# Performance work log

Measured on AMD Instinct MI355X. Metric: run time of the kernel, lower is better.

## Reference

```python
import jax, jax.numpy as jnp
import numpy as np

N = 100000      # nodes
E = 6400000     # edges (avg degree 64)
S = 8           # FSM states
X = 2 ** S      # neighborhood 'characters' (256)
ITERS = 20      # NeuralFSM.iterations


def setup_inputs() -> dict:
    key = jax.random.key(0)
    k1, k2, k3 = jax.random.split(key, 3)
    # one-hot initial node states [N, S]
    state_idx = jax.random.randint(k1, (N,), 0, S)
    s0 = jax.nn.one_hot(state_idx, S, dtype=jnp.float32)
    # edge list [2, E]
    edge_index = jax.random.randint(k2, (2, E), 0, N, dtype=jnp.int32)
    # FSM transition tensor T[char, state, :] is one-hot over next state -> [X, S, S]
    next_state = jax.random.randint(k3, (X, S), 0, S)
    T = jax.nn.one_hot(next_state, S, dtype=jnp.float32)
    return {"s0": s0, "edge_index": edge_index, "T": T}


def reference(s0, edge_index, T):
    n_nodes, n_states = s0.shape
    src, dst = edge_index[0], edge_index[1]
    powers = (2 ** jnp.arange(n_states)).astype(jnp.int32)  # base-2 encoding of thresholded aggr

    def step(s, _):
        # message = x_j gathered from source nodes, scatter-added at destinations
        msg_sum = jax.ops.segment_sum(s[src], dst, num_segments=n_nodes)  # [N, S]
        # threshold (> 0.5) then clamp to {0,1}
        aggr = (msg_sum > 0.5).astype(jnp.int32)                          # [N, S]
        # multiple-hot -> index into 2^S characters (one-hot folded into a gather)
        idx = aggr @ powers                                               # [N]
        # einsum('x,s,xst->t') with one-hot char == gather T[idx] then contract state
        new_s = jnp.einsum('ns,nst->nt', s, T[idx])                       # [N, S]
        return new_s, None

    s_final, _ = jax.lax.scan(step, s0, None, length=ITERS)
    return s_final
```

## Files before the change

kernel.cpp:

```cpp
#include <hip/hip_runtime.h>
#include <hip/hip_bf16.h>
#include <stdint.h>


#define NN 100000
#define EE 6400000
#define NCHARS 2048
#define ITERS 20
#define NB_NODE 391

#define NBKT 250
#define NPB 400
#define WPS 12500
#define X4N 3125
#define CEDGE 12800
#define NCHUNK 500
#define PCAP 13312

#define BLINES 25
#define BAR_ARR(i) ((i) * 16)
#define BAR_TOP    800
#define BAR_REL(i) (832 + (i) * 16)
#define BAR_WORDS  2048

typedef uint32_t u32x4 __attribute__((ext_vector_type(4)));

__global__ void init_kernel(uint32_t* __restrict__ bar, uint32_t* __restrict__ gPk0) {
    int i = blockIdx.x * blockDim.x + threadIdx.x;
    int stride = gridDim.x * blockDim.x;
    for (int j = i; j < BAR_WORDS; j += stride) bar[j] = 0u;
    for (int j = i; j < WPS; j += stride) gPk0[j] = 0u;
}

__global__ void decode_kernel(const float* __restrict__ s0,
                              const float* __restrict__ T,
                              uint32_t* __restrict__ gPk0,
                              uint8_t* __restrict__ nextT) {
    int i = blockIdx.x * blockDim.x + threadIdx.x;
    if (i < NCHARS) {
        const float* row = T + i * 8;
        int t = 0;
        #pragma unroll
        for (int k = 1; k < 8; ++k) if (row[k] > 0.5f) t = k;
        nextT[i] = (uint8_t)t;
    }
    if (i < NN) {
        const float* row = s0 + i * 8;
        int s = 0;
        #pragma unroll
        for (int k = 1; k < 8; ++k) if (row[k] > 0.5f) s = k;
        atomicOr(&gPk0[i >> 3], (uint32_t)s << ((i & 7) << 2));
    }
}

__global__ void __launch_bounds__(512) p1_hist(const int* __restrict__ dst,
                                               uint32_t* __restrict__ hist) {
    __shared__ uint32_t cnt[NBKT];
    int t = threadIdx.x;
    int c = blockIdx.x;
    for (int i = t; i < NBKT; i += 512) cnt[i] = 0;
    __syncthreads();
    int e0 = c * CEDGE;
    for (int i = t; i < CEDGE; i += 512) atomicAdd(&cnt[dst[e0 + i] / NPB], 1u);
    __syncthreads();
    for (int i = t; i < NBKT; i += 512) hist[(size_t)c * NBKT + i] = cnt[i];
}

__global__ void p2a_scan(uint32_t* __restrict__ hist, uint32_t* __restrict__ total) {
    __shared__ uint32_t lds[256];
    int t = threadIdx.x;
    int b = blockIdx.x;
    uint32_t carry = 0;
    for (int c0 = 0; c0 < NCHUNK; c0 += 256) {
        int c = c0 + t;
        uint32_t v = (c < NCHUNK) ? hist[(size_t)c * NBKT + b] : 0u;
        lds[t] = v;
        __syncthreads();
        for (int off = 1; off < 256; off <<= 1) {
            uint32_t x = (t >= off) ? lds[t - off] : 0u;
            __syncthreads();
            lds[t] += x;
            __syncthreads();
        }
        if (c < NCHUNK) hist[(size_t)c * NBKT + b] = lds[t] - v + carry;
        uint32_t tot = lds[255];
        __syncthreads();
        carry += tot;
    }
    if (t == 0) total[b] = carry;
}

__global__ void p2b_scan(const uint32_t* __restrict__ total,
                         uint32_t* __restrict__ bucket_base) {
    __shared__ uint32_t lds[512];
    int t = threadIdx.x;
    uint32_t v = (t < NBKT) ? total[t] : 0u;
    lds[t] = v;
    __syncthreads();
    for (int off = 1; off < 512; off <<= 1) {
        uint32_t x = (t >= off) ? lds[t - off] : 0u;
        __syncthreads();
        lds[t] += x;
        __syncthreads();
    }
    if (t < NBKT) bucket_base[t] = lds[t] - v;
    if (t == 511) bucket_base[NBKT] = lds[511];
}

__global__ void __launch_bounds__(512) p3_partition(const int* __restrict__ src,
                                                    const int* __restrict__ dst,
                                                    const uint32_t* __restrict__ hist,
                                                    const uint32_t* __restrict__ bucket_base,
                                                    uint32_t* __restrict__ csr) {
    __shared__ uint32_t stage[CEDGE];
    __shared__ uint32_t loc[NBKT + 1];
    __shared__ uint32_t cur[NBKT];
    __shared__ uint32_t scanb[512];
    int t = threadIdx.x;
    int c = blockIdx.x;
    int e0 = c * CEDGE;
    for (int i = t; i < NBKT; i += 512) cur[i] = 0;
    __syncthreads();
    for (int i = t; i < CEDGE; i += 512) atomicAdd(&cur[dst[e0 + i] / NPB], 1u);
    __syncthreads();
    uint32_t v = (t < NBKT) ? cur[t] : 0u;
    scanb[t] = v;
    __syncthreads();
    for (int off = 1; off < 512; off <<= 1) {
        uint32_t x = (t >= off) ? scanb[t - off] : 0u;
        __syncthreads();
        scanb[t] += x;
        __syncthreads();
    }
    if (t < NBKT) { loc[t] = scanb[t] - v; cur[t] = scanb[t] - v; }
    if (t == 0) loc[NBKT] = CEDGE;
    __syncthreads();
    for (int i = t; i < CEDGE; i += 512) {
        int d = dst[e0 + i];
        int s = src[e0 + i];
        int bb = d / NPB;
        uint32_t dl = (uint32_t)(d - bb * NPB);
        uint32_t pos = atomicAdd(&cur[bb], 1u);
        stage[pos] = ((uint32_t)s << 9) | dl;
    }
    __syncthreads();
    if (t < NBKT) cur[t] = bucket_base[t] + hist[(size_t)c * NBKT + t] - loc[t];
    __syncthreads();
    for (int i = t; i < CEDGE; i += 512) {
        int lo = 0, hi = NBKT;
        while (hi - lo > 1) { int mid = (lo + hi) >> 1; if (loc[mid] <= (uint32_t)i) lo = mid; else hi = mid; }
        csr[cur[lo] + (uint32_t)i] = stage[i];
    }
}

__global__ void __launch_bounds__(512) p4_sortsrc(uint32_t* __restrict__ csr,
                                                  const uint32_t* __restrict__ bucket_base) {
    __shared__ uint32_t st[PCAP];
    __shared__ uint32_t binh[512];
    int t = threadIdx.x;
    int j = blockIdx.x;
    int b = j >> 1, h = j & 1;
    uint32_t base = bucket_base[b], endb = bucket_base[b + 1];
    uint32_t n = endb - base;
    uint32_t n1 = (n + 1) >> 1;
    uint32_t r0 = h ? base + n1 : base;
    uint32_t cnt = h ? n - n1 : n1;
    if (cnt > PCAP) return;
    for (uint32_t i = t; i < cnt; i += 512) st[i] = csr[r0 + i];
    binh[t] = 0;
    __syncthreads();
    for (uint32_t i = t; i < cnt; i += 512) atomicAdd(&binh[st[i] >> 17], 1u);
    __syncthreads();
    uint32_t v = binh[t];
    __syncthreads();
    for (int off = 1; off < 512; off <<= 1) {
        uint32_t x = (t >= off) ? binh[t - off] : 0u;
        __syncthreads();
        binh[t] += x;
        __syncthreads();
    }
    uint32_t excl = binh[t] - v;
    __syncthreads();
    binh[t] = excl;
    __syncthreads();
    for (uint32_t i = t; i < cnt; i += 512) {
        uint32_t w = st[i];
        uint32_t pos = atomicAdd(&binh[w >> 17], 1u);
        csr[r0 + pos] = w;
    }
}

__global__ void __launch_bounds__(1024) mega_kernel(const uint32_t* __restrict__ csr,
                                                    const uint32_t* __restrict__ bucket_base,
                                                    uint32_t* __restrict__ gPkA,
                                                    uint32_t* __restrict__ gPkB,
                                                    const uint8_t* __restrict__ nextT,
                                                    float* __restrict__ out,
                                                    uint32_t* __restrict__ bar) {
    __shared__ uint32_t sPk[WPS];
    __shared__ uint32_t mask[NPB];
    __shared__ uint32_t packOwn[NPB / 8];
    __shared__ uint8_t  nT[NCHARS];
    __shared__ uint8_t  sown[NPB];
    int t = threadIdx.x;
    int b = blockIdx.x;
    uint32_t base = bucket_base[b];
    uint32_t end  = bucket_base[b + 1];

    if (t < 512) ((uint32_t*)nT)[t] = ((const uint32_t*)nextT)[t];
    const int line = b % BLINES;

    for (int p = 0; p < ITERS; ++p) {
        const uint32_t* curG = (p & 1) ? gPkB : gPkA;
        uint32_t*       nxtG = (p & 1) ? gPkA : gPkB;
        {
            const u32x4* g4 = (const u32x4*)curG;
            int i0 = t, i1 = t + 1024, i2 = t + 2048;
            int i3 = t + 3072; if (i3 > X4N - 1) i3 = X4N - 1;
            const u32x4 *p0 = g4 + i0, *p1 = g4 + i1, *p2 = g4 + i2, *p3 = g4 + i3;
            u32x4 a0, a1, a2, a3;
            asm volatile(
                "global_load_dwordx4 %0, %4, off sc1\n\t"
                "global_load_dwordx4 %1, %5, off sc1\n\t"
                "global_load_dwordx4 %2, %6, off sc1\n\t"
                "global_load_dwordx4 %3, %7, off sc1\n\t"
                "s_waitcnt vmcnt(0)"
                : "=&v"(a0), "=&v"(a1), "=&v"(a2), "=&v"(a3)
                : "v"(p0), "v"(p1), "v"(p2), "v"(p3)
                : "memory");
            u32x4* s4 = (u32x4*)sPk;
            s4[i0] = a0; s4[i1] = a1; s4[i2] = a2; s4[i3] = a3;
        }
        if (t < NPB) mask[t] = 0;
        if (t < NPB / 8) packOwn[t] = 0;
        __syncthreads();

        uint32_t e = base + t;
        for (; e + 3072 < end; e += 4096) {
            uint32_t w0 = csr[e], w1 = csr[e + 1024], w2 = csr[e + 2048], w3 = csr[e + 3072];
            uint32_t s0_ = w0 >> 9, s1_ = w1 >> 9, s2_ = w2 >> 9, s3_ = w3 >> 9;
            uint32_t n0 = (sPk[s0_ >> 3] >> ((s0_ & 7) << 2)) & 7u;
            uint32_t n1 = (sPk[s1_ >> 3] >> ((s1_ & 7) << 2)) & 7u;
            uint32_t n2 = (sPk[s2_ >> 3] >> ((s2_ & 7) << 2)) & 7u;
            uint32_t n3 = (sPk[s3_ >> 3] >> ((s3_ & 7) << 2)) & 7u;
            atomicOr(&mask[w0 & 511u], 1u << n0);
            atomicOr(&mask[w1 & 511u], 1u << n1);
            atomicOr(&mask[w2 & 511u], 1u << n2);
            atomicOr(&mask[w3 & 511u], 1u << n3);
        }
        for (; e < end; e += 1024) {
            uint32_t w = csr[e];
            uint32_t s_ = w >> 9;
            uint32_t nb = (sPk[s_ >> 3] >> ((s_ & 7) << 2)) & 7u;
            atomicOr(&mask[w & 511u], 1u << nb);
        }
        __syncthreads();

        if (t < NPB) {
            int node = b * NPB + t;
            uint32_t sOwn = (sPk[node >> 3] >> ((node & 7) << 2)) & 7u;
            uint8_t ns = nT[(mask[t] << 3) + sOwn];
            sown[t] = ns;
            atomicOr(&packOwn[t >> 3], (uint32_t)ns << ((t & 7) << 2));
        }
        __syncthreads();
        if (p < ITERS - 1) {
            if (t < NPB / 8)
                __hip_atomic_store(&nxtG[(NPB / 8) * b + t], packOwn[t],
                                   __ATOMIC_RELAXED, __HIP_MEMORY_SCOPE_AGENT);
            __syncthreads();
            if (t == 0) {
                uint32_t epoch = (uint32_t)(p + 1);
                uint32_t old = atomicAdd(&bar[BAR_ARR(line)], 1u);
                if (old + 1u == 10u * epoch) {
                    uint32_t told = atomicAdd(&bar[BAR_TOP], 1u);
                    if (told + 1u == (uint32_t)BLINES * epoch) {
                        for (int r = 0; r < BLINES; ++r)
                            atomicExch(&bar[BAR_REL(r)], epoch);
                    }
                }
                while (__hip_atomic_load(&bar[BAR_REL(line)], __ATOMIC_RELAXED,
                                         __HIP_MEMORY_SCOPE_AGENT) < epoch)
                    __builtin_amdgcn_s_sleep(16);
            }
            __syncthreads();
        }
    }
    __syncthreads();
    for (int f = t; f < NPB * 8; f += 1024) {
        int node = f >> 3;
        out[(size_t)b * (NPB * 8) + f] = ((f & 7) == (int)sown[node]) ? 1.f : 0.f;
    }
}

__global__ void fb_decode(const float* __restrict__ s0, const float* __restrict__ T,
                          uint8_t* __restrict__ state, uint8_t* __restrict__ nextT,
                          uint32_t* __restrict__ mask) {
    int i = blockIdx.x * blockDim.x + threadIdx.x;
    if (i < NCHARS) {
        const float* row = T + i * 8;
        int t = 0;
        #pragma unroll
        for (int k = 1; k < 8; ++k) if (row[k] > 0.5f) t = k;
        nextT[i] = (uint8_t)t;
    }
    if (i < NN) {
        const float* row = s0 + i * 8;
        int s = 0;
        #pragma unroll
        for (int k = 1; k < 8; ++k) if (row[k] > 0.5f) s = k;
        state[i] = (uint8_t)s;
        mask[i] = 0u;
    }
}
__global__ void fb_edge(const int* __restrict__ src, const int* __restrict__ dst,
                        const uint8_t* __restrict__ state, uint32_t* __restrict__ mask) {
    int i = blockIdx.x * blockDim.x + threadIdx.x;
    int stride = gridDim.x * blockDim.x;
    for (int e = i; e < EE; e += stride) atomicOr(&mask[dst[e]], 1u << state[src[e]]);
}
__global__ void fb_update(uint8_t* __restrict__ state, uint32_t* __restrict__ mask,
                          const uint8_t* __restrict__ nextT) {
    int i = blockIdx.x * blockDim.x + threadIdx.x;
    if (i < NN) {
        uint32_t m = mask[i];
        state[i] = nextT[(m << 3) + state[i]];
        mask[i] = 0u;
    }
}
__global__ void fb_output(const uint8_t* __restrict__ state, float* __restrict__ out) {
    int i = blockIdx.x * blockDim.x + threadIdx.x;
    if (i < NN) {
        int s = state[i];
        float4 lo = make_float4(s == 0 ? 1.f : 0.f, s == 1 ? 1.f : 0.f,
                                s == 2 ? 1.f : 0.f, s == 3 ? 1.f : 0.f);
        float4 hi = make_float4(s == 4 ? 1.f : 0.f, s == 5 ? 1.f : 0.f,
                                s == 6 ? 1.f : 0.f, s == 7 ? 1.f : 0.f);
        float4* o = (float4*)(out + (size_t)i * 8);
        o[0] = lo;
        o[1] = hi;
    }
}

extern "C" void kernel_launch(void* const* d_in, const int* in_sizes, int n_in,
                              void* d_out, int out_size, void* d_ws, size_t ws_size,
                              hipStream_t stream) {
    const float* s0  = (const float*)d_in[0];
    const int*   ei  = (const int*)d_in[1];
    const float* T   = (const float*)d_in[2];
    float*       out = (float*)d_out;
    const int* src = ei;
    const int* dst = ei + EE;

    uint8_t* basep = (uint8_t*)d_ws;
    size_t off = 0;
    auto alloc = [&](size_t sz) -> void* {
        void* p = basep + off;
        off += (sz + 255) & ~(size_t)255;
        return p;
    };
    uint32_t* csr         = (uint32_t*)alloc(sizeof(uint32_t) * EE);
    uint32_t* hist        = (uint32_t*)alloc(sizeof(uint32_t) * (size_t)NCHUNK * NBKT);
    uint32_t* total       = (uint32_t*)alloc(sizeof(uint32_t) * NBKT);
    uint32_t* bucket_base = (uint32_t*)alloc(sizeof(uint32_t) * (NBKT + 1));
    uint8_t*  nextT       = (uint8_t*)alloc(NCHARS);
    uint32_t* gPkA        = (uint32_t*)alloc(sizeof(uint32_t) * WPS);
    uint32_t* gPkB        = (uint32_t*)alloc(sizeof(uint32_t) * WPS);
    uint32_t* bar         = (uint32_t*)alloc(sizeof(uint32_t) * BAR_WORDS);
    bool have_ws = (off <= ws_size);

    if (have_ws) {
        init_kernel<<<58, 256, 0, stream>>>(bar, gPkA);
        decode_kernel<<<NB_NODE, 256, 0, stream>>>(s0, T, gPkA, nextT);
        p1_hist<<<NCHUNK, 512, 0, stream>>>(dst, hist);
        p2a_scan<<<NBKT, 256, 0, stream>>>(hist, total);
        p2b_scan<<<1, 512, 0, stream>>>(total, bucket_base);
        p3_partition<<<NCHUNK, 512, 0, stream>>>(src, dst, hist, bucket_base, csr);
        p4_sortsrc<<<NBKT * 2, 512, 0, stream>>>(csr, bucket_base);
        mega_kernel<<<NBKT, 1024, 0, stream>>>(csr, bucket_base, gPkA, gPkB,
                                               nextT, out, bar);
    } else {
        uint32_t* mask = (uint32_t*)d_ws;
        uint8_t*  nT   = (uint8_t*)d_ws + 400128;
        uint8_t*  st   = (uint8_t*)d_ws + 402432;
        fb_decode<<<NB_NODE, 256, 0, stream>>>(s0, T, st, nT, mask);
        for (int it = 0; it < ITERS; ++it) {
            fb_edge<<<2048, 256, 0, stream>>>(src, dst, st, mask);
            fb_update<<<NB_NODE, 256, 0, stream>>>(st, mask, nT);
        }
        fb_output<<<NB_NODE, 256, 0, stream>>>(st, out);
    }
}
```

Baseline: 305.7 us.

## Fuse init into decode, use per-wave LDS histograms and vectorized edge loads

Merges init_kernel into decode_kernel so one thread packs eight node states per word, which removes the global atomicOr and the separate zeroing launch. p1_hist and p3_partition now read dst/src as int4 and count into per-wavefront LDS histograms. This spreads contention on the shared-memory atomics. p3 derives per-wave scatter offsets from a prefix over those histograms and drops the second cursor reset. The cost is more LDS per block, and the staged order within a bucket changes, which p4's sort handles.

```diff
diff --git a/kernel.cpp b/kernel.cpp
--- a/kernel.cpp
+++ b/kernel.cpp
@@ -7,7 +7,6 @@
 #define EE 6400000
 #define NCHARS 2048
 #define ITERS 20
-#define NB_NODE 391
 
 #define NBKT 250
 #define NPB 400
@@ -25,18 +24,14 @@
 
 typedef uint32_t u32x4 __attribute__((ext_vector_type(4)));
 
-__global__ void init_kernel(uint32_t* __restrict__ bar, uint32_t* __restrict__ gPk0) {
+__global__ void decode_kernel(const float* __restrict__ s0,
+                              const float* __restrict__ T,
+                              uint32_t* __restrict__ gPk0,
+                              uint8_t* __restrict__ nextT,
+                              uint32_t* __restrict__ bar) {
     int i = blockIdx.x * blockDim.x + threadIdx.x;
     int stride = gridDim.x * blockDim.x;
     for (int j = i; j < BAR_WORDS; j += stride) bar[j] = 0u;
-    for (int j = i; j < WPS; j += stride) gPk0[j] = 0u;
-}
-
-__global__ void decode_kernel(const float* __restrict__ s0,
-                              const float* __restrict__ T,
-                              uint32_t* __restrict__ gPk0,
-                              uint8_t* __restrict__ nextT) {
-    int i = blockIdx.x * blockDim.x + threadIdx.x;
     if (i < NCHARS) {
         const float* row = T + i * 8;
         int t = 0;
@@ -44,26 +39,43 @@
         for (int k = 1; k < 8; ++k) if (row[k] > 0.5f) t = k;
         nextT[i] = (uint8_t)t;
     }
-    if (i < NN) {
-        const float* row = s0 + i * 8;
-        int s = 0;
-        #pragma unroll
-        for (int k = 1; k < 8; ++k) if (row[k] > 0.5f) s = k;
-        atomicOr(&gPk0[i >> 3], (uint32_t)s << ((i & 7) << 2));
+    for (int j = i; j < WPS; j += stride) {
+        uint32_t wv = 0;
+        const float* rows = s0 + (size_t)j * 64;
+        #pragma unroll
+        for (int k = 0; k < 8; ++k) {
+            const float* row = rows + k * 8;
+            int s = 0;
+            #pragma unroll
+            for (int q = 1; q < 8; ++q) if (row[q] > 0.5f) s = q;
+            wv |= (uint32_t)s << (k << 2);
+        }
+        gPk0[j] = wv;
     }
 }
 
 __global__ void __launch_bounds__(512) p1_hist(const int* __restrict__ dst,
                                                uint32_t* __restrict__ hist) {
-    __shared__ uint32_t cnt[NBKT];
-    int t = threadIdx.x;
+    __shared__ uint32_t cw[8][256];
+    int t = threadIdx.x, w = t >> 6;
     int c = blockIdx.x;
-    for (int i = t; i < NBKT; i += 512) cnt[i] = 0;
-    __syncthreads();
-    int e0 = c * CEDGE;
-    for (int i = t; i < CEDGE; i += 512) atomicAdd(&cnt[dst[e0 + i] / NPB], 1u);
-    __syncthreads();
-    for (int i = t; i < NBKT; i += 512) hist[(size_t)c * NBKT + i] = cnt[i];
+    for (int i = t; i < 8 * 256; i += 512) ((uint32_t*)cw)[i] = 0;
+    __syncthreads();
+    const int4* p = (const int4*)(dst + c * CEDGE);
+    for (int i = t; i < CEDGE / 4; i += 512) {
+        int4 d = p[i];
+        atomicAdd(&cw[w][d.x / NPB], 1u);
+        atomicAdd(&cw[w][d.y / NPB], 1u);
+        atomicAdd(&cw[w][d.z / NPB], 1u);
+        atomicAdd(&cw[w][d.w / NPB], 1u);
+    }
+    __syncthreads();
+    for (int b = t; b < NBKT; b += 512) {
+        uint32_t s = 0;
+        #pragma unroll
+        for (int w2 = 0; w2 < 8; ++w2) s += cw[w2][b];
+        hist[(size_t)c * NBKT + b] = s;
+    }
 }
 
 __global__ void p2a_scan(uint32_t* __restrict__ hist, uint32_t* __restrict__ total) {
@@ -113,18 +125,31 @@
                                                     const uint32_t* __restrict__ bucket_base,
                                                     uint32_t* __restrict__ csr) {
     __shared__ uint32_t stage[CEDGE];
+    __shared__ uint32_t cw[8][256];
     __shared__ uint32_t loc[NBKT + 1];
-    __shared__ uint32_t cur[NBKT];
+    __shared__ uint32_t segoff[NBKT];
     __shared__ uint32_t scanb[512];
-    int t = threadIdx.x;
+    int t = threadIdx.x, w = t >> 6;
     int c = blockIdx.x;
     int e0 = c * CEDGE;
-    for (int i = t; i < NBKT; i += 512) cur[i] = 0;
-    __syncthreads();
-    for (int i = t; i < CEDGE; i += 512) atomicAdd(&cur[dst[e0 + i] / NPB], 1u);
-    __syncthreads();
-    uint32_t v = (t < NBKT) ? cur[t] : 0u;
-    scanb[t] = v;
+    const int4* ps4 = (const int4*)(src + e0);
+    const int4* pd4 = (const int4*)(dst + e0);
+    for (int i = t; i < 8 * 256; i += 512) ((uint32_t*)cw)[i] = 0;
+    __syncthreads();
+    for (int i = t; i < CEDGE / 4; i += 512) {
+        int4 d = pd4[i];
+        atomicAdd(&cw[w][d.x / NPB], 1u);
+        atomicAdd(&cw[w][d.y / NPB], 1u);
+        atomicAdd(&cw[w][d.z / NPB], 1u);
+        atomicAdd(&cw[w][d.w / NPB], 1u);
+    }
+    __syncthreads();
+    uint32_t tot = 0;
+    if (t < NBKT) {
+        #pragma unroll
+        for (int w2 = 0; w2 < 8; ++w2) tot += cw[w2][t];
+    }
+    scanb[t] = tot;
     __syncthreads();
     for (int off = 1; off < 512; off <<= 1) {
         uint32_t x = (t >= off) ? scanb[t - off] : 0u;
@@ -132,24 +157,38 @@
         scanb[t] += x;
         __syncthreads();
     }
-    if (t < NBKT) { loc[t] = scanb[t] - v; cur[t] = scanb[t] - v; }
+    if (t < NBKT) {
+        uint32_t excl = scanb[t] - tot;
+        loc[t] = excl;
+        segoff[t] = bucket_base[t] + hist[(size_t)c * NBKT + t] - excl;
+        uint32_t acc = excl;
+        #pragma unroll
+        for (int w2 = 0; w2 < 8; ++w2) {
+            uint32_t cv = cw[w2][t];
+            cw[w2][t] = acc;
+            acc += cv;
+        }
+    }
     if (t == 0) loc[NBKT] = CEDGE;
     __syncthreads();
-    for (int i = t; i < CEDGE; i += 512) {
-        int d = dst[e0 + i];
-        int s = src[e0 + i];
-        int bb = d / NPB;
-        uint32_t dl = (uint32_t)(d - bb * NPB);
-        uint32_t pos = atomicAdd(&cur[bb], 1u);
-        stage[pos] = ((uint32_t)s << 9) | dl;
-    }
-    __syncthreads();
-    if (t < NBKT) cur[t] = bucket_base[t] + hist[(size_t)c * NBKT + t] - loc[t];
+    for (int i = t; i < CEDGE / 4; i += 512) {
+        int4 d = pd4[i];
+        int4 s = ps4[i];
+        int bb; uint32_t dl, pos;
+        bb = d.x / NPB; dl = (uint32_t)(d.x - bb * NPB);
+        pos = atomicAdd(&cw[w][bb], 1u); stage[pos] = ((uint32_t)s.x << 9) | dl;
+        bb = d.y / NPB; dl = (uint32_t)(d.y - bb * NPB);
+        pos = atomicAdd(&cw[w][bb], 1u); stage[pos] = ((uint32_t)s.y << 9) | dl;
+        bb = d.z / NPB; dl = (uint32_t)(d.z - bb * NPB);
+        pos = atomicAdd(&cw[w][bb], 1u); stage[pos] = ((uint32_t)s.z << 9) | dl;
+        bb = d.w / NPB; dl = (uint32_t)(d.w - bb * NPB);
+        pos = atomicAdd(&cw[w][bb], 1u); stage[pos] = ((uint32_t)s.w << 9) | dl;
+    }
     __syncthreads();
     for (int i = t; i < CEDGE; i += 512) {
         int lo = 0, hi = NBKT;
         while (hi - lo > 1) { int mid = (lo + hi) >> 1; if (loc[mid] <= (uint32_t)i) lo = mid; else hi = mid; }
-        csr[cur[lo] + (uint32_t)i] = stage[i];
+        csr[segoff[lo] + (uint32_t)i] = stage[i];
     }
 }
 
@@ -370,8 +409,7 @@
     bool have_ws = (off <= ws_size);
 
     if (have_ws) {
-        init_kernel<<<58, 256, 0, stream>>>(bar, gPkA);
-        decode_kernel<<<NB_NODE, 256, 0, stream>>>(s0, T, gPkA, nextT);
+        decode_kernel<<<51, 256, 0, stream>>>(s0, T, gPkA, nextT, bar);
         p1_hist<<<NCHUNK, 512, 0, stream>>>(dst, hist);
         p2a_scan<<<NBKT, 256, 0, stream>>>(hist, total);
         p2b_scan<<<1, 512, 0, stream>>>(total, bucket_base);
@@ -383,11 +421,11 @@
         uint32_t* mask = (uint32_t*)d_ws;
         uint8_t*  nT   = (uint8_t*)d_ws + 400128;
         uint8_t*  st   = (uint8_t*)d_ws + 402432;
-        fb_decode<<<NB_NODE, 256, 0, stream>>>(s0, T, st, nT, mask);
+        fb_decode<<<391, 256, 0, stream>>>(s0, T, st, nT, mask);
         for (int it = 0; it < ITERS; ++it) {
             fb_edge<<<2048, 256, 0, stream>>>(src, dst, st, mask);
-            fb_update<<<NB_NODE, 256, 0, stream>>>(st, mask, nT);
-        }
-        fb_output<<<NB_NODE, 256, 0, stream>>>(st, out);
-    }
-}
+            fb_update<<<391, 256, 0, stream>>>(st, mask, nT);
+        }
+        fb_output<<<391, 256, 0, stream>>>(st, out);
+    }
+}
```

Result: faster. 284.9 us (-6.8%).
